# Optimization experiments

Measured on AMD Instinct MI355X. Metric: run time of the kernel, lower is better.

Reference implementation:

```python
import jax, jax.numpy as jnp
import numpy as np

D_MODEL = 1024
NUM_HEADS = 16
THETA = 10000.0
BATCH = 2
SEQ = 2048


def _rope(x, pos, theta):
    # x: (b, h, l, d), pos: (l,)
    d = x.shape[-1]
    half = d // 2
    inv_freq = theta ** (-(jnp.arange(half, dtype=x.dtype) / half))  # theta^(-2k/d)
    ang = pos.astype(x.dtype)[:, None] * inv_freq[None, :]  # (l, half)
    cos, sin = jnp.cos(ang), jnp.sin(ang)
    x1, x2 = x[..., ::2], x[..., 1::2]
    r1 = x1 * cos - x2 * sin
    r2 = x1 * sin + x2 * cos
    return jnp.stack([r1, r2], axis=-1).reshape(x.shape)


def setup_inputs() -> dict:
    key = jax.random.key(0)
    k1, k2, k3 = jax.random.split(key, 3)
    x = jax.random.normal(k1, (BATCH, SEQ, D_MODEL), dtype=jnp.float32)
    W_kqv = jax.random.normal(k2, (3 * D_MODEL, D_MODEL), dtype=jnp.float32) * (1.0 / np.sqrt(D_MODEL))
    W_o = jax.random.normal(k3, (D_MODEL, D_MODEL), dtype=jnp.float32) * (1.0 / np.sqrt(D_MODEL))
    return {"x": x, "W_kqv": W_kqv, "W_o": W_o}


def reference(x, W_kqv, W_o):
    b, L, _ = x.shape
    h = NUM_HEADS
    d = D_MODEL // h
    kqv = x @ W_kqv.T  # (b, l, 3*d_model)
    K, Q, V = jnp.split(kqv, 3, axis=-1)  # chunk order in source: K, Q, V
    # (b, l, h*d) -> (b, h, l, d)
    Q = Q.reshape(b, L, h, d).transpose(0, 2, 1, 3)
    K = K.reshape(b, L, h, d).transpose(0, 2, 1, 3)
    V = V.reshape(b, L, h, d).transpose(0, 2, 1, 3)
    pos = jnp.arange(L)
    Q = _rope(Q, pos, THETA)
    K = _rope(K, pos, THETA)
    scores = jnp.einsum('bhqd,bhkd->bhqk', Q, K) / jnp.sqrt(jnp.asarray(d, x.dtype))
    causal = jnp.tril(jnp.ones((L, L), dtype=bool))
    scores = jnp.where(causal, scores, jnp.finfo(scores.dtype).min)
    probs = jax.nn.softmax(scores, axis=-1)
    out = jnp.einsum('bhqk,bhkd->bhqd', probs, V)
    out = out.transpose(0, 2, 1, 3).reshape(b, L, h * d)
    return out @ W_o.T
```

## Files before the change

kernel.cpp:

```cpp
#include <hip/hip_runtime.h>
#include <hip/hip_bf16.h>
#include <stdint.h>

#define BATCH 2
#define SEQ 2048
#define DMODEL 1024
#define NHEADS 16
#define HDIM 64
#define MROWS (BATCH*SEQ)
#define N3 (3*DMODEL)
#define NSLOT 80

typedef __attribute__((ext_vector_type(8))) __bf16 bf16x8;
typedef __attribute__((ext_vector_type(4))) float f32x4;

__device__ __forceinline__ ushort f2b(float f) {
  uint32_t u = __builtin_bit_cast(uint32_t, f);
  uint32_t r = (u + 0x7FFFu + ((u >> 16) & 1u)) >> 16;
  return (ushort)r;
}
__device__ __forceinline__ float b2f(ushort h) {
  return __builtin_bit_cast(float, (uint32_t)h << 16);
}
__device__ __forceinline__ float exp2_hw(float x) {
  float r;
  asm("v_exp_f32 %0, %1" : "=v"(r) : "v"(x));
  return r;
}
__device__ __forceinline__ uint32_t cvtpk(float a, float b) {
  uint32_t r;
  asm("v_cvt_pk_bf16_f32 %0, %1, %2" : "=v"(r) : "v"(a), "v"(b));
  return r;
}

__global__ void f2b3_kernel(const float* __restrict__ a, const float* __restrict__ b,
                            const float* __restrict__ c,
                            ushort* __restrict__ oa, ushort* __restrict__ ob,
                            ushort* __restrict__ oc, int na, int nb, int nc) {
  int i = blockIdx.x * blockDim.x + threadIdx.x;
  const float* src; ushort* dst; int off;
  if (i < na)           { src = a; dst = oa; off = i; }
  else if (i < na + nb) { src = b; dst = ob; off = i - na; }
  else if (i < na + nb + nc) { src = c; dst = oc; off = i - na - nb; }
  else return;
  float4 v = ((const float4*)src)[off];
  uint32_t lo = cvtpk(v.x, v.y), hi_ = cvtpk(v.z, v.w);
  ((uint2*)dst)[off] = make_uint2(lo, hi_);
}

template<int OUTF>
__global__ __launch_bounds__(256)
void gemm_bt(const ushort* __restrict__ A, const ushort* __restrict__ Bw,
             void* __restrict__ Cv, int M, int N, int K) {
  __shared__ __align__(16) ushort As[128*32];
  __shared__ __align__(16) ushort Bs[128*32];
  const int tid  = threadIdx.x;
  const int wid  = tid >> 6;
  const int lane = tid & 63;
  const int wr   = wid >> 1, wc = wid & 1;
  const int l16  = lane & 15, lhi = lane >> 4;
  const int nb   = N >> 7;
  const int brow = (blockIdx.x / nb) << 7;
  const int bcol = (blockIdx.x % nb) << 7;

  f32x4 acc[4][4] = {};

  for (int k0 = 0; k0 < K; k0 += 32) {
    __syncthreads();
#pragma unroll
    for (int it = 0; it < 2; ++it) {
      const int cb    = (wid * 2 + it) * 64;
      const int chunk = cb + lane;
      const int r     = chunk >> 2;
      const int c8    = chunk & 3;
      const ushort* ga = A  + (size_t)(brow + r) * K + k0 + c8 * 8;
      const ushort* gb = Bw + (size_t)(bcol + r) * K + k0 + c8 * 8;
      __builtin_amdgcn_global_load_lds(
          (const __attribute__((address_space(1))) void*)ga,
          (__attribute__((address_space(3))) void*)(As + cb * 8), 16, 0, 0);
      __builtin_amdgcn_global_load_lds(
          (const __attribute__((address_space(1))) void*)gb,
          (__attribute__((address_space(3))) void*)(Bs + cb * 8), 16, 0, 0);
    }
    __syncthreads();

    bf16x8 af[4], bfr[4];
#pragma unroll
    for (int m = 0; m < 4; ++m)
      af[m] = *(const bf16x8*)(As + (wr*64 + m*16 + l16)*32 + lhi*8);
#pragma unroll
    for (int n = 0; n < 4; ++n)
      bfr[n] = *(const bf16x8*)(Bs + (wc*64 + n*16 + l16)*32 + lhi*8);
#pragma unroll
    for (int m = 0; m < 4; ++m)
#pragma unroll
      for (int n = 0; n < 4; ++n)
        acc[m][n] = __builtin_amdgcn_mfma_f32_16x16x32_bf16(af[m], bfr[n], acc[m][n], 0, 0, 0);
  }

#pragma unroll
  for (int m = 0; m < 4; ++m)
#pragma unroll
    for (int n = 0; n < 4; ++n)
#pragma unroll
      for (int r = 0; r < 4; ++r) {
        const int row = brow + wr*64 + m*16 + lhi*4 + r;
        const int col = bcol + wc*64 + n*16 + l16;
        if (OUTF) ((float*)Cv)[(size_t)row * N + col] = acc[m][n][r];
        else      ((ushort*)Cv)[(size_t)row * N + col] = f2b(acc[m][n][r]);
      }
}

__global__ void rope_kernel(const ushort* __restrict__ kqv,
                            ushort* __restrict__ qb, ushort* __restrict__ kb) {
  const float SC = 0.18033688011112042f;
  int idx = blockIdx.x * blockDim.x + threadIdx.x;
  int i  = idx & 31;
  int h  = (idx >> 5) & 15;
  int bl = idx >> 9;
  int l  = bl & (SEQ - 1);
  int b  = bl >> 11;
  float inv = exp2f((float)i * -0.4152410118609203f);
  float ang = (float)l * inv;
  float s, c;
  sincosf(ang, &s, &c);
  size_t base = (size_t)bl * N3 + h * HDIM + 2 * i;
  uint32_t kp = *(const uint32_t*)(kqv + base);
  uint32_t qp = *(const uint32_t*)(kqv + base + DMODEL);
  float k1 = b2f((ushort)(kp & 0xffff)), k2 = b2f((ushort)(kp >> 16));
  float q1 = b2f((ushort)(qp & 0xffff)), q2 = b2f((ushort)(qp >> 16));
  float kr1 = k1 * c - k2 * s, kr2 = k1 * s + k2 * c;
  float qr1 = (q1 * c - q2 * s) * SC, qr2 = (q1 * s + q2 * c) * SC;
  size_t ob = ((size_t)(b * NHEADS + h) * SEQ + l) * HDIM + 2 * i;
  *(uint32_t*)(kb + ob) = cvtpk(kr1, kr2);
  *(uint32_t*)(qb + ob) = cvtpk(qr1, qr2);
}

__global__ void vtrans_kernel(const ushort* __restrict__ kqv, ushort* __restrict__ vt) {
  __shared__ ushort tile[64][65];
  int bid = blockIdx.x;
  int lt = bid & 31, bh = bid >> 5;
  int b = bh >> 4, h = bh & 15;
  int tid = threadIdx.x;
  int r = tid >> 2, cq = tid & 3;
  size_t gbase = ((size_t)(b * SEQ + lt * 64 + r)) * N3 + 2 * DMODEL + h * HDIM + cq * 16;
#pragma unroll
  for (int j = 0; j < 16; ++j) tile[r][cq * 16 + j] = kqv[gbase + j];
  __syncthreads();
  int d = tid >> 2;
  size_t obase = ((size_t)(bh * HDIM + d)) * SEQ + lt * 64 + cq * 16;
#pragma unroll
  for (int j = 0; j < 16; ++j) vt[obase + j] = tile[cq * 16 + j][d];
}

__global__ __launch_bounds__(256, 4)
void attn_part_kernel(const ushort* __restrict__ qb, const ushort* __restrict__ kb,
                      const ushort* __restrict__ vt,
                      ushort* __restrict__ po, float* __restrict__ pm, float* __restrict__ pl) {
  __shared__ __align__(16) ushort Kbuf[2][4096];
  __shared__ __align__(16) ushort Vbuf[2][4096];
  __shared__ __align__(16) ushort plds[4][1024];
  int bid = blockIdx.x;
  int bh = bid & 31;
  int slot = bid >> 5;
  int band = (slot < 8) ? 0 : (slot < 24) ? 1 : (slot < 48) ? 2 : 3;
  const int offb0 = (band == 0) ? 0 : (band == 1) ? 8 : (band == 2) ? 24 : 48;
  int s0i = slot - offb0;
  int qt = band * 8 + s0i / (band + 1);
  int c  = s0i % (band + 1);
  int kt0   = c * 8;
  int ktend = min(kt0 + 8, qt + 1);

  int wid = threadIdx.x >> 6, lane = threadIdx.x & 63;
  int l16 = lane & 15, lhi = lane >> 4;
  int r0 = qt * 64 + wid * 16;

  const ushort* Q  = qb + (size_t)bh * SEQ * HDIM;
  const ushort* Kp = kb + (size_t)bh * SEQ * HDIM;
  const ushort* Vp = vt + (size_t)bh * HDIM * SEQ;

  bf16x8 qf[2];
#pragma unroll
  for (int kc = 0; kc < 2; ++kc)
    qf[kc] = *(const bf16x8*)(Q + (size_t)(r0 + l16) * HDIM + kc * 32 + lhi * 8);

  float mq = -3.0e38f, lsq = 0.0f;
  f32x4 o[4] = {};

  char* pbase = (char*)&plds[wid][0];
  const int swz = (l16 & 7) << 4;

  auto STAGE = [&](int buf, int kt) {
    ushort* kd = &Kbuf[buf][0];
    ushort* vd = &Vbuf[buf][0];
    const ushort* kg = Kp + (size_t)kt * 64 * HDIM;
    const ushort* vg = Vp + kt * 64;
#pragma unroll
    for (int it = 0; it < 2; ++it) {
      const int cb = it * 256 + wid * 64;
      const int ci = cb + lane;
      const int row = ci >> 3;
      const int sl  = (ci & 7) ^ (row & 7);
      __builtin_amdgcn_global_load_lds(
          (const __attribute__((address_space(1))) void*)(kg + row * HDIM + sl * 8),
          (__attribute__((address_space(3))) void*)(kd + cb * 8), 16, 0, 0);
      __builtin_amdgcn_global_load_lds(
          (const __attribute__((address_space(1))) void*)(vg + (size_t)row * SEQ + sl * 8),
          (__attribute__((address_space(3))) void*)(vd + cb * 8), 16, 0, 0);
    }
  };

  int cur = 0;
  STAGE(0, kt0);
  __syncthreads();

  for (int kt = kt0; kt < ktend; ++kt) {
    if (kt + 1 < ktend) STAGE(cur ^ 1, kt + 1);

    const char* kc_ = (const char*)&Kbuf[cur][0];
    const char* vc_ = (const char*)&Vbuf[cur][0];

    f32x4 s[4];
#pragma unroll
    for (int n = 0; n < 4; ++n) {
      const int kvr = n * 16 + l16;
      bf16x8 kf0 = *(const bf16x8*)(kc_ + kvr*128 + ((lhi     ^ (kvr&7)) * 16));
      bf16x8 kf1 = *(const bf16x8*)(kc_ + kvr*128 + (((4+lhi) ^ (kvr&7)) * 16));
      f32x4 z = 0.0f;
      z = __builtin_amdgcn_mfma_f32_16x16x32_bf16(kf0, qf[0], z, 0, 0, 0);
      z = __builtin_amdgcn_mfma_f32_16x16x32_bf16(kf1, qf[1], z, 0, 0, 0);
      s[n] = z;
    }

    if (kt == qt) {
#pragma unroll
      for (int n = 0; n < 4; ++n)
#pragma unroll
        for (int r = 0; r < 4; ++r)
          if (kt*64 + n*16 + lhi*4 + r > r0 + l16) s[n][r] = -3.0e38f;
    }

    float t0 = fmaxf(fmaxf(s[0][0], s[0][1]), fmaxf(s[0][2], s[0][3]));
    float t1 = fmaxf(fmaxf(s[1][0], s[1][1]), fmaxf(s[1][2], s[1][3]));
    float t2 = fmaxf(fmaxf(s[2][0], s[2][1]), fmaxf(s[2][2], s[2][3]));
    float t3 = fmaxf(fmaxf(s[3][0], s[3][1]), fmaxf(s[3][2], s[3][3]));
    float pmx = fmaxf(fmaxf(t0, t1), fmaxf(t2, t3));
    pmx = fmaxf(pmx, __shfl_xor(pmx, 16));
    pmx = fmaxf(pmx, __shfl_xor(pmx, 32));

    if (!__all(pmx <= mq)) {
      float mn = fmaxf(mq, pmx);
      float alpha = exp2_hw(mq - mn);
      mq = mn;
      lsq *= alpha;
      float alphaT[4];
#pragma unroll
      for (int r = 0; r < 4; ++r)
        alphaT[r] = __shfl(alpha, lhi * 4 + r);
#pragma unroll
      for (int f = 0; f < 4; ++f)
#pragma unroll
        for (int r = 0; r < 4; ++r)
          o[f][r] *= alphaT[r];
    }

    float ps = 0.0f;
#pragma unroll
    for (int n = 0; n < 4; ++n)
#pragma unroll
      for (int r = 0; r < 4; ++r) {
        float p = exp2_hw(s[n][r] - mq);
        s[n][r] = p;
        ps += p;
      }
    ps += __shfl_xor(ps, 16);
    ps += __shfl_xor(ps, 32);
    lsq += ps;

#pragma unroll
    for (int n = 0; n < 4; ++n) {
      uint32_t w0 = cvtpk(s[n][0], s[n][1]);
      uint32_t w1 = cvtpk(s[n][2], s[n][3]);
      int kvloc = n*16 + lhi*4;
      *(uint32_t*)(pbase + ((l16*128 + kvloc*2) ^ swz))       = w0;
      *(uint32_t*)(pbase + ((l16*128 + (kvloc+2)*2) ^ swz))   = w1;
    }
    bf16x8 pa0 = *(const bf16x8*)(pbase + ((l16*128 + 0*64 + lhi*16) ^ swz));
    bf16x8 pa1 = *(const bf16x8*)(pbase + ((l16*128 + 1*64 + lhi*16) ^ swz));

#pragma unroll
    for (int f = 0; f < 4; ++f) {
      const int dr = f * 16 + l16;
      bf16x8 vf0 = *(const bf16x8*)(vc_ + dr*128 + ((lhi     ^ (dr&7)) * 16));
      bf16x8 vf1 = *(const bf16x8*)(vc_ + dr*128 + (((4+lhi) ^ (dr&7)) * 16));
      o[f] = __builtin_amdgcn_mfma_f32_16x16x32_bf16(pa0, vf0, o[f], 0, 0, 0);
      o[f] = __builtin_amdgcn_mfma_f32_16x16x32_bf16(pa1, vf1, o[f], 0, 0, 0);
    }

    __syncthreads();
    cur ^= 1;
  }

  size_t pb = (size_t)bh * NSLOT + slot;
  if (lhi == 0) {
    pm[pb * 64 + wid * 16 + l16] = mq;
    pl[pb * 64 + wid * 16 + l16] = lsq;
  }
  int qlr = wid * 16 + lhi * 4;
#pragma unroll
  for (int r = 0; r < 4; ++r)
#pragma unroll
    for (int f = 0; f < 4; ++f)
      po[pb * 4096 + (size_t)(qlr + r) * 64 + f*16 + l16] = f2b(o[f][r]);
}

__global__ __launch_bounds__(256)
void attn_merge_kernel(const ushort* __restrict__ po, const float* __restrict__ pm,
                       const float* __restrict__ pl, ushort* __restrict__ attn) {
  int bid = blockIdx.x;
  int bh = bid & 31, qt = bid >> 5;
  int band = qt >> 3;
  int nc = band + 1;
  int off = band * (band + 1) * 4 + (qt & 7) * (band + 1);
  size_t sbase = (size_t)bh * NSLOT + off;
  int t = threadIdx.x;
  int r = t >> 2, cg = t & 3;

  float mv[4], w[4];
  float M = -3.0e38f;
#pragma unroll
  for (int ci = 0; ci < 4; ++ci) {
    mv[ci] = (ci < nc) ? pm[(sbase + ci) * 64 + r] : -3.0e38f;
    M = fmaxf(M, mv[ci]);
  }
  float L = 0.0f;
#pragma unroll
  for (int ci = 0; ci < 4; ++ci) {
    w[ci] = (ci < nc) ? exp2f(mv[ci] - M) : 0.0f;
    if (ci < nc) L += w[ci] * pl[(sbase + ci) * 64 + r];
  }
  float acc[16] = {};
#pragma unroll
  for (int ci = 0; ci < 4; ++ci) {
    if (ci < nc) {
      const ushort* op = po + (sbase + ci) * 4096 + (size_t)r * 64 + cg * 16;
      uint4 v0 = *(const uint4*)op;
      uint4 v1 = *(const uint4*)(op + 8);
      const uint32_t uu[8] = {v0.x, v0.y, v0.z, v0.w, v1.x, v1.y, v1.z, v1.w};
#pragma unroll
      for (int j = 0; j < 8; ++j) {
        acc[2*j]   += w[ci] * b2f((ushort)(uu[j] & 0xffff));
        acc[2*j+1] += w[ci] * b2f((ushort)(uu[j] >> 16));
      }
    }
  }
  float invL = 1.0f / L;
  int b = bh >> 4, h = bh & 15;
  size_t ob = ((size_t)(b * SEQ + qt * 64 + r)) * DMODEL + h * 64 + cg * 16;
  uint32_t packed[8];
#pragma unroll
  for (int j = 0; j < 8; ++j)
    packed[j] = cvtpk(acc[2*j] * invL, acc[2*j+1] * invL);
  *(uint4*)(attn + ob)     = make_uint4(packed[0], packed[1], packed[2], packed[3]);
  *(uint4*)(attn + ob + 8) = make_uint4(packed[4], packed[5], packed[6], packed[7]);
}

extern "C" void kernel_launch(void* const* d_in, const int* in_sizes, int n_in,
                              void* d_out, int out_size, void* d_ws, size_t ws_size,
                              hipStream_t stream) {
  const float* x    = (const float*)d_in[0];
  const float* wkqv = (const float*)d_in[1];
  const float* wo   = (const float*)d_in[2];
  float* out = (float*)d_out;

  ushort* xb   = (ushort*)d_ws;
  ushort* wkb  = xb  + (size_t)MROWS * DMODEL;
  ushort* wob  = wkb + (size_t)N3 * DMODEL;
  ushort* kqv  = wob + (size_t)DMODEL * DMODEL;
  ushort* qb   = kqv + (size_t)MROWS * N3;
  ushort* kb   = qb  + (size_t)MROWS * DMODEL;
  ushort* vt   = kb  + (size_t)MROWS * DMODEL;
  ushort* attn = xb;

  ushort* po = kqv;
  float*  pmv = (float*)(kqv + (size_t)32 * NSLOT * 4096);
  float*  plv = pmv + (size_t)32 * NSLOT * 64;

  int nx = MROWS * DMODEL / 4, nw = N3 * DMODEL / 4, no = DMODEL * DMODEL / 4;
  f2b3_kernel<<<(nx + nw + no) / 256, 256, 0, stream>>>(x, wkqv, wo, xb, wkb, wob, nx, nw, no);

  gemm_bt<0><<<(MROWS/128) * (N3/128), 256, 0, stream>>>(xb, wkb, (void*)kqv, MROWS, N3, DMODEL);

  rope_kernel<<<(MROWS * NHEADS * 32) / 256, 256, 0, stream>>>(kqv, qb, kb);
  vtrans_kernel<<<BATCH * NHEADS * (SEQ / 64), 256, 0, stream>>>(kqv, vt);

  attn_part_kernel<<<32 * NSLOT, 256, 0, stream>>>(qb, kb, vt, po, pmv, plv);
  attn_merge_kernel<<<32 * 32, 256, 0, stream>>>(po, pmv, plv, attn);

  gemm_bt<1><<<(MROWS/128) * (DMODEL/128), 256, 0, stream>>>(attn, wob, (void*)out, MROWS, DMODEL, DMODEL);
}
```

Baseline: 134.8 us.

## Replace split-KV attention with paired-query-tile blocks and fuse prep kernels

Attention no longer splits each query tile's causal range into KV chunks with a separate merge pass. Each block now pairs query tile p with tile 31-p so every block does the same amount of work, shares each staged K/V tile between both queries, and normalizes and writes the output directly. This removes the partial-output writes, the merge kernel and one launch. The rope and V-transpose kernels are merged into a single launch. The cost is only 512 blocks with higher register pressure (launch bounds now 2), which may leave the GPU underoccupied compared with the 2560 split blocks.

```diff
diff --git a/kernel.cpp b/kernel.cpp
--- a/kernel.cpp
+++ b/kernel.cpp
@@ -9,7 +9,6 @@
 #define HDIM 64
 #define MROWS (BATCH*SEQ)
 #define N3 (3*DMODEL)
-#define NSLOT 80
 
 typedef __attribute__((ext_vector_type(8))) __bf16 bf16x8;
 typedef __attribute__((ext_vector_type(4))) float f32x4;
@@ -111,81 +110,78 @@
       }
 }
 
-__global__ void rope_kernel(const ushort* __restrict__ kqv,
-                            ushort* __restrict__ qb, ushort* __restrict__ kb) {
-  const float SC = 0.18033688011112042f;
-  int idx = blockIdx.x * blockDim.x + threadIdx.x;
-  int i  = idx & 31;
-  int h  = (idx >> 5) & 15;
-  int bl = idx >> 9;
-  int l  = bl & (SEQ - 1);
-  int b  = bl >> 11;
-  float inv = exp2f((float)i * -0.4152410118609203f);
-  float ang = (float)l * inv;
-  float s, c;
-  sincosf(ang, &s, &c);
-  size_t base = (size_t)bl * N3 + h * HDIM + 2 * i;
-  uint32_t kp = *(const uint32_t*)(kqv + base);
-  uint32_t qp = *(const uint32_t*)(kqv + base + DMODEL);
-  float k1 = b2f((ushort)(kp & 0xffff)), k2 = b2f((ushort)(kp >> 16));
-  float q1 = b2f((ushort)(qp & 0xffff)), q2 = b2f((ushort)(qp >> 16));
-  float kr1 = k1 * c - k2 * s, kr2 = k1 * s + k2 * c;
-  float qr1 = (q1 * c - q2 * s) * SC, qr2 = (q1 * s + q2 * c) * SC;
-  size_t ob = ((size_t)(b * NHEADS + h) * SEQ + l) * HDIM + 2 * i;
-  *(uint32_t*)(kb + ob) = cvtpk(kr1, kr2);
-  *(uint32_t*)(qb + ob) = cvtpk(qr1, qr2);
-}
-
-__global__ void vtrans_kernel(const ushort* __restrict__ kqv, ushort* __restrict__ vt) {
+__global__ __launch_bounds__(256)
+void prep_kernel(const ushort* __restrict__ kqv,
+                 ushort* __restrict__ qb, ushort* __restrict__ kb, ushort* __restrict__ vt) {
   __shared__ ushort tile[64][65];
-  int bid = blockIdx.x;
-  int lt = bid & 31, bh = bid >> 5;
-  int b = bh >> 4, h = bh & 15;
-  int tid = threadIdx.x;
-  int r = tid >> 2, cq = tid & 3;
-  size_t gbase = ((size_t)(b * SEQ + lt * 64 + r)) * N3 + 2 * DMODEL + h * HDIM + cq * 16;
-#pragma unroll
-  for (int j = 0; j < 16; ++j) tile[r][cq * 16 + j] = kqv[gbase + j];
-  __syncthreads();
-  int d = tid >> 2;
-  size_t obase = ((size_t)(bh * HDIM + d)) * SEQ + lt * 64 + cq * 16;
-#pragma unroll
-  for (int j = 0; j < 16; ++j) vt[obase + j] = tile[cq * 16 + j][d];
-}
-
-__global__ __launch_bounds__(256, 4)
-void attn_part_kernel(const ushort* __restrict__ qb, const ushort* __restrict__ kb,
-                      const ushort* __restrict__ vt,
-                      ushort* __restrict__ po, float* __restrict__ pm, float* __restrict__ pl) {
+  if (blockIdx.x < 1024) {
+    int bid = blockIdx.x;
+    int lt = bid & 31, bh = bid >> 5;
+    int b = bh >> 4, h = bh & 15;
+    int tid = threadIdx.x;
+    int r = tid >> 2, cq = tid & 3;
+    size_t gbase = ((size_t)(b * SEQ + lt * 64 + r)) * N3 + 2 * DMODEL + h * HDIM + cq * 16;
+#pragma unroll
+    for (int j = 0; j < 16; ++j) tile[r][cq * 16 + j] = kqv[gbase + j];
+    __syncthreads();
+    int d = tid >> 2;
+    size_t obase = ((size_t)(bh * HDIM + d)) * SEQ + lt * 64 + cq * 16;
+#pragma unroll
+    for (int j = 0; j < 16; ++j) vt[obase + j] = tile[cq * 16 + j][d];
+  } else {
+    const float SC = 0.18033688011112042f;
+    int idx = (blockIdx.x - 1024) * 256 + threadIdx.x;
+    int i  = idx & 31;
+    int h  = (idx >> 5) & 15;
+    int bl = idx >> 9;
+    int l  = bl & (SEQ - 1);
+    int b  = bl >> 11;
+    float inv = exp2f((float)i * -0.4152410118609203f);
+    float ang = (float)l * inv;
+    float s, c;
+    sincosf(ang, &s, &c);
+    size_t base = (size_t)bl * N3 + h * HDIM + 2 * i;
+    uint32_t kp = *(const uint32_t*)(kqv + base);
+    uint32_t qp = *(const uint32_t*)(kqv + base + DMODEL);
+    float k1 = b2f((ushort)(kp & 0xffff)), k2 = b2f((ushort)(kp >> 16));
+    float q1 = b2f((ushort)(qp & 0xffff)), q2 = b2f((ushort)(qp >> 16));
+    float kr1 = k1 * c - k2 * s, kr2 = k1 * s + k2 * c;
+    float qr1 = (q1 * c - q2 * s) * SC, qr2 = (q1 * s + q2 * c) * SC;
+    size_t ob = ((size_t)(b * NHEADS + h) * SEQ + l) * HDIM + 2 * i;
+    *(uint32_t*)(kb + ob) = cvtpk(kr1, kr2);
+    *(uint32_t*)(qb + ob) = cvtpk(qr1, qr2);
+  }
+}
+
+__global__ __launch_bounds__(256, 2)
+void attn_kernel(const ushort* __restrict__ qb, const ushort* __restrict__ kb,
+                 const ushort* __restrict__ vt, ushort* __restrict__ ao) {
   __shared__ __align__(16) ushort Kbuf[2][4096];
   __shared__ __align__(16) ushort Vbuf[2][4096];
   __shared__ __align__(16) ushort plds[4][1024];
-  int bid = blockIdx.x;
-  int bh = bid & 31;
-  int slot = bid >> 5;
-  int band = (slot < 8) ? 0 : (slot < 24) ? 1 : (slot < 48) ? 2 : 3;
-  const int offb0 = (band == 0) ? 0 : (band == 1) ? 8 : (band == 2) ? 24 : 48;
-  int s0i = slot - offb0;
-  int qt = band * 8 + s0i / (band + 1);
-  int c  = s0i % (band + 1);
-  int kt0   = c * 8;
-  int ktend = min(kt0 + 8, qt + 1);
-
-  int wid = threadIdx.x >> 6, lane = threadIdx.x & 63;
-  int l16 = lane & 15, lhi = lane >> 4;
-  int r0 = qt * 64 + wid * 16;
+  const int bid = blockIdx.x;
+  const int bh = bid & 31;
+  const int p  = bid >> 5;
+  const int qtA = p, qtB = 31 - p;
+
+  const int wid = threadIdx.x >> 6, lane = threadIdx.x & 63;
+  const int l16 = lane & 15, lhi = lane >> 4;
+  const int r0A = qtA * 64 + wid * 16;
+  const int r0B = qtB * 64 + wid * 16;
 
   const ushort* Q  = qb + (size_t)bh * SEQ * HDIM;
   const ushort* Kp = kb + (size_t)bh * SEQ * HDIM;
   const ushort* Vp = vt + (size_t)bh * HDIM * SEQ;
 
-  bf16x8 qf[2];
-#pragma unroll
-  for (int kc = 0; kc < 2; ++kc)
-    qf[kc] = *(const bf16x8*)(Q + (size_t)(r0 + l16) * HDIM + kc * 32 + lhi * 8);
-
-  float mq = -3.0e38f, lsq = 0.0f;
-  f32x4 o[4] = {};
+  bf16x8 qfA[2], qfB[2];
+#pragma unroll
+  for (int kc = 0; kc < 2; ++kc) {
+    qfA[kc] = *(const bf16x8*)(Q + (size_t)(r0A + l16) * HDIM + kc * 32 + lhi * 8);
+    qfB[kc] = *(const bf16x8*)(Q + (size_t)(r0B + l16) * HDIM + kc * 32 + lhi * 8);
+  }
+
+  float mqA = -3.0e38f, lsA = 0.0f, mqB = -3.0e38f, lsB = 0.0f;
+  f32x4 oA[4] = {}, oB[4] = {};
 
   char* pbase = (char*)&plds[wid][0];
   const int swz = (l16 & 7) << 4;
@@ -210,16 +206,8 @@
     }
   };
 
-  int cur = 0;
-  STAGE(0, kt0);
-  __syncthreads();
-
-  for (int kt = kt0; kt < ktend; ++kt) {
-    if (kt + 1 < ktend) STAGE(cur ^ 1, kt + 1);
-
-    const char* kc_ = (const char*)&Kbuf[cur][0];
-    const char* vc_ = (const char*)&Vbuf[cur][0];
-
+  auto BODY = [&](const char* kc_, const char* vc_, bf16x8 (&qf)[2],
+                  float& mq, float& lsq, f32x4 (&o)[4], int r0, int qt, int kt) {
     f32x4 s[4];
 #pragma unroll
     for (int n = 0; n < 4; ++n) {
@@ -231,7 +219,6 @@
       z = __builtin_amdgcn_mfma_f32_16x16x32_bf16(kf1, qf[1], z, 0, 0, 0);
       s[n] = z;
     }
-
     if (kt == qt) {
 #pragma unroll
       for (int n = 0; n < 4; ++n)
@@ -239,7 +226,6 @@
         for (int r = 0; r < 4; ++r)
           if (kt*64 + n*16 + lhi*4 + r > r0 + l16) s[n][r] = -3.0e38f;
     }
-
     float t0 = fmaxf(fmaxf(s[0][0], s[0][1]), fmaxf(s[0][2], s[0][3]));
     float t1 = fmaxf(fmaxf(s[1][0], s[1][1]), fmaxf(s[1][2], s[1][3]));
     float t2 = fmaxf(fmaxf(s[2][0], s[2][1]), fmaxf(s[2][2], s[2][3]));
@@ -269,9 +255,9 @@
     for (int n = 0; n < 4; ++n)
 #pragma unroll
       for (int r = 0; r < 4; ++r) {
-        float p = exp2_hw(s[n][r] - mq);
-        s[n][r] = p;
-        ps += p;
+        float pv = exp2_hw(s[n][r] - mq);
+        s[n][r] = pv;
+        ps += pv;
       }
     ps += __shfl_xor(ps, 16);
     ps += __shfl_xor(ps, 32);
@@ -296,73 +282,37 @@
       o[f] = __builtin_amdgcn_mfma_f32_16x16x32_bf16(pa0, vf0, o[f], 0, 0, 0);
       o[f] = __builtin_amdgcn_mfma_f32_16x16x32_bf16(pa1, vf1, o[f], 0, 0, 0);
     }
-
+  };
+
+  int cur = 0;
+  STAGE(0, 0);
+  __syncthreads();
+
+  for (int kt = 0; kt <= qtB; ++kt) {
+    if (kt < qtB) STAGE(cur ^ 1, kt + 1);
+    const char* kc_ = (const char*)&Kbuf[cur][0];
+    const char* vc_ = (const char*)&Vbuf[cur][0];
+    BODY(kc_, vc_, qfB, mqB, lsB, oB, r0B, qtB, kt);
+    if (kt <= qtA)
+      BODY(kc_, vc_, qfA, mqA, lsA, oA, r0A, qtA, kt);
     __syncthreads();
     cur ^= 1;
   }
 
-  size_t pb = (size_t)bh * NSLOT + slot;
-  if (lhi == 0) {
-    pm[pb * 64 + wid * 16 + l16] = mq;
-    pl[pb * 64 + wid * 16 + l16] = lsq;
-  }
-  int qlr = wid * 16 + lhi * 4;
-#pragma unroll
-  for (int r = 0; r < 4; ++r)
-#pragma unroll
-    for (int f = 0; f < 4; ++f)
-      po[pb * 4096 + (size_t)(qlr + r) * 64 + f*16 + l16] = f2b(o[f][r]);
-}
-
-__global__ __launch_bounds__(256)
-void attn_merge_kernel(const ushort* __restrict__ po, const float* __restrict__ pm,
-                       const float* __restrict__ pl, ushort* __restrict__ attn) {
-  int bid = blockIdx.x;
-  int bh = bid & 31, qt = bid >> 5;
-  int band = qt >> 3;
-  int nc = band + 1;
-  int off = band * (band + 1) * 4 + (qt & 7) * (band + 1);
-  size_t sbase = (size_t)bh * NSLOT + off;
-  int t = threadIdx.x;
-  int r = t >> 2, cg = t & 3;
-
-  float mv[4], w[4];
-  float M = -3.0e38f;
-#pragma unroll
-  for (int ci = 0; ci < 4; ++ci) {
-    mv[ci] = (ci < nc) ? pm[(sbase + ci) * 64 + r] : -3.0e38f;
-    M = fmaxf(M, mv[ci]);
-  }
-  float L = 0.0f;
-#pragma unroll
-  for (int ci = 0; ci < 4; ++ci) {
-    w[ci] = (ci < nc) ? exp2f(mv[ci] - M) : 0.0f;
-    if (ci < nc) L += w[ci] * pl[(sbase + ci) * 64 + r];
-  }
-  float acc[16] = {};
-#pragma unroll
-  for (int ci = 0; ci < 4; ++ci) {
-    if (ci < nc) {
-      const ushort* op = po + (sbase + ci) * 4096 + (size_t)r * 64 + cg * 16;
-      uint4 v0 = *(const uint4*)op;
-      uint4 v1 = *(const uint4*)(op + 8);
-      const uint32_t uu[8] = {v0.x, v0.y, v0.z, v0.w, v1.x, v1.y, v1.z, v1.w};
-#pragma unroll
-      for (int j = 0; j < 8; ++j) {
-        acc[2*j]   += w[ci] * b2f((ushort)(uu[j] & 0xffff));
-        acc[2*j+1] += w[ci] * b2f((ushort)(uu[j] >> 16));
-      }
-    }
-  }
-  float invL = 1.0f / L;
-  int b = bh >> 4, h = bh & 15;
-  size_t ob = ((size_t)(b * SEQ + qt * 64 + r)) * DMODEL + h * 64 + cg * 16;
-  uint32_t packed[8];
-#pragma unroll
-  for (int j = 0; j < 8; ++j)
-    packed[j] = cvtpk(acc[2*j] * invL, acc[2*j+1] * invL);
-  *(uint4*)(attn + ob)     = make_uint4(packed[0], packed[1], packed[2], packed[3]);
-  *(uint4*)(attn + ob + 8) = make_uint4(packed[4], packed[5], packed[6], packed[7]);
+  const int b = bh >> 4, h = bh & 15;
+  float invA = 1.0f / lsA, invB = 1.0f / lsB;
+#pragma unroll
+  for (int r = 0; r < 4; ++r) {
+    float wA = __shfl(invA, lhi * 4 + r);
+    float wB = __shfl(invB, lhi * 4 + r);
+    size_t baseA = ((size_t)(b * SEQ + r0A + lhi*4 + r)) * DMODEL + h * HDIM + l16;
+    size_t baseB = ((size_t)(b * SEQ + r0B + lhi*4 + r)) * DMODEL + h * HDIM + l16;
+#pragma unroll
+    for (int f = 0; f < 4; ++f) {
+      ao[baseA + f*16] = f2b(oA[f][r] * wA);
+      ao[baseB + f*16] = f2b(oB[f][r] * wB);
+    }
+  }
 }
 
 extern "C" void kernel_launch(void* const* d_in, const int* in_sizes, int n_in,
@@ -382,20 +332,14 @@
   ushort* vt   = kb  + (size_t)MROWS * DMODEL;
   ushort* attn = xb;
 
-  ushort* po = kqv;
-  float*  pmv = (float*)(kqv + (size_t)32 * NSLOT * 4096);
-  float*  plv = pmv + (size_t)32 * NSLOT * 64;
-
   int nx = MROWS * DMODEL / 4, nw = N3 * DMODEL / 4, no = DMODEL * DMODEL / 4;
   f2b3_kernel<<<(nx + nw + no) / 256, 256, 0, stream>>>(x, wkqv, wo, xb, wkb, wob, nx, nw, no);
 
   gemm_bt<0><<<(MROWS/128) * (N3/128), 256, 0, stream>>>(xb, wkb, (void*)kqv, MROWS, N3, DMODEL);
 
-  rope_kernel<<<(MROWS * NHEADS * 32) / 256, 256, 0, stream>>>(kqv, qb, kb);
-  vtrans_kernel<<<BATCH * NHEADS * (SEQ / 64), 256, 0, stream>>>(kqv, vt);
-
-  attn_part_kernel<<<32 * NSLOT, 256, 0, stream>>>(qb, kb, vt, po, pmv, plv);
-  attn_merge_kernel<<<32 * 32, 256, 0, stream>>>(po, pmv, plv, attn);
+  prep_kernel<<<1024 + (MROWS * NHEADS * 32) / 256, 256, 0, stream>>>(kqv, qb, kb, vt);
+
+  attn_kernel<<<512, 256, 0, stream>>>(qb, kb, vt, attn);
 
   gemm_bt<1><<<(MROWS/128) * (DMODEL/128), 256, 0, stream>>>(attn, wob, (void*)out, MROWS, DMODEL, DMODEL);
 }
```

Measured after the change: 126.6 us. 6.1% less time.
